# Kernel optimization log

Measured on AMD Instinct MI355X. Metric: run time of the kernel, lower is better.

Reference implementation:

```python
import jax, jax.numpy as jnp
import numpy as np

N, F = 8192, 64
SLOPE = 3.0


def _mlp(h, params):
    # params: list of (W[in,out], b[out]); Tanh after EVERY linear (incl. last)
    for W, b in params:
        h = jnp.tanh(h @ W + b)
    return h


def setup_inputs() -> dict:
    key = jax.random.key(0)
    ks = jax.random.split(key, 16)
    x = jax.random.normal(ks[0], (N, F, 2), dtype=jnp.float32)
    def lin(k, fi, fo):
        k1, k2 = jax.random.split(k)
        s = 1.0 / np.sqrt(fi)
        W = jax.random.uniform(k1, (fi, fo), jnp.float32, -s, s)
        b = jax.random.uniform(k2, (fo,), jnp.float32, -s, s)
        return W, b
    w_in1, b_in1 = lin(ks[1], 2, 4)
    w_in2, b_in2 = lin(ks[2], 4, 4)
    w_in3, b_in3 = lin(ks[3], 4, 1)
    w_a1, b_a1 = lin(ks[4], 1, 2)
    w_a2, b_a2 = lin(ks[5], 2, 1)
    w_b1, b_b1 = lin(ks[6], 1, 2)
    w_b2, b_b2 = lin(ks[7], 2, 1)
    return dict(x=x,
                w_in1=w_in1, b_in1=b_in1, w_in2=w_in2, b_in2=b_in2,
                w_in3=w_in3, b_in3=b_in3,
                w_a1=w_a1, b_a1=b_a1, w_a2=w_a2, b_a2=b_a2,
                w_b1=w_b1, b_b1=b_b1, w_b2=w_b2, b_b2=b_b2)


def reference(x, w_in1, b_in1, w_in2, b_in2, w_in3, b_in3,
              w_a1, b_a1, w_a2, b_a2, w_b1, b_b1, w_b2, b_b2):
    n, f = x.shape[0], x.shape[1]
    # per-coordinate-pair encode: [N*F,2] -> [N*F,1] -> [N,F]
    h = _mlp(x.reshape(-1, 2), [(w_in1, b_in1), (w_in2, b_in2), (w_in3, b_in3)])
    xe = h.reshape(n, f)
    # dense self-attention aggregation, softmax over dim 0 (columns normalized)
    attn = jax.nn.softmax(xe @ xe.T, axis=0)  # [N,N]
    xe = attn @ xe                            # [N,F]
    # pairwise squared euclidean distances E[i,j] = ||x_i - x_j||^2
    sq = jnp.sum(xe * xe, axis=1)             # [N]
    E = sq[:, None] + sq[None, :] - 2.0 * (xe @ xe.T)
    m = jnp.mean(E).reshape(1)                # [1]
    alpha = jnp.exp(SLOPE * _mlp(m, [(w_a1, b_a1), (w_a2, b_a2)]))
    beta = jnp.exp(-SLOPE * _mlp(m, [(w_b1, b_b1), (w_b2, b_b2)]))
    return xe, alpha, beta
```

## Files before the change

kernel.cpp:

```cpp
#include <hip/hip_runtime.h>
#include <cstdint>

typedef __bf16 bf16x8 __attribute__((ext_vector_type(8)));
typedef __bf16 bf16x4 __attribute__((ext_vector_type(4)));
typedef float  f32x4  __attribute__((ext_vector_type(4)));

#define N_PTS 8192
#define FDIM  64
#define NF    (N_PTS * FDIM)

__device__ __forceinline__ float ftanh(float x) {
    float e = __expf(2.f * x);
    return 1.f - 2.f / (e + 1.f);
}

__global__ __launch_bounds__(256) void k_encode(
    const float* __restrict__ x,
    const float* __restrict__ w1, const float* __restrict__ b1,
    const float* __restrict__ w2, const float* __restrict__ b2,
    const float* __restrict__ w3, const float* __restrict__ b3,
    __bf16* __restrict__ xe)
{
    int idx = blockIdx.x * 256 + threadIdx.x;
    float2 p = ((const float2*)x)[idx];
    float h1[4], h2[4];
#pragma unroll
    for (int o = 0; o < 4; o++)
        h1[o] = ftanh(p.x * w1[o] + p.y * w1[4 + o] + b1[o]);
#pragma unroll
    for (int o = 0; o < 4; o++) {
        float s = b2[o];
#pragma unroll
        for (int i = 0; i < 4; i++) s += h1[i] * w2[i * 4 + o];
        h2[o] = ftanh(s);
    }
    float s3 = b3[0];
#pragma unroll
    for (int i = 0; i < 4; i++) s3 += h2[i] * w3[i];
    xe[idx] = (__bf16)ftanh(s3);
}

__global__ __launch_bounds__(256) void k_pass1(
    const __bf16* __restrict__ xe, float* __restrict__ Dp)
{
    __shared__ __bf16 sI[128 * 72];
    const int tid = threadIdx.x;
    const int j0 = blockIdx.x * 64;
    const int ibase = blockIdx.y * 1024;
    const int wave = tid >> 6, lane = tid & 63, c = lane & 15, q = lane >> 4;

    bf16x8 Bf[4][2];
#pragma unroll
    for (int jt = 0; jt < 4; jt++)
#pragma unroll
        for (int kc = 0; kc < 2; kc++)
            Bf[jt][kc] = *(const bf16x8*)(xe + (j0 + 16 * jt + c) * 64 + kc * 32 + q * 8);

    float es[4] = {0.f, 0.f, 0.f, 0.f};
    for (int ic = 0; ic < 8; ic++) {
        __syncthreads();
#pragma unroll
        for (int k = 0; k < 4; k++) {
            int seg = tid + k * 256; int r = seg >> 3, c8 = seg & 7;
            *(uint4*)(sI + r * 72 + c8 * 8) =
                *(const uint4*)(xe + (ibase + ic * 128 + r) * 64 + c8 * 8);
        }
        __syncthreads();
#pragma unroll
        for (int g = 0; g < 2; g++) {
            bf16x8 a0 = *(const bf16x8*)(sI + (32 * wave + 16 * g + c) * 72 + q * 8);
            bf16x8 a1 = *(const bf16x8*)(sI + (32 * wave + 16 * g + c) * 72 + 32 + q * 8);
#pragma unroll
            for (int jt = 0; jt < 4; jt++) {
                f32x4 s = {0.f, 0.f, 0.f, 0.f};
                s = __builtin_amdgcn_mfma_f32_16x16x32_bf16(a0, Bf[jt][0], s, 0, 0, 0);
                s = __builtin_amdgcn_mfma_f32_16x16x32_bf16(a1, Bf[jt][1], s, 0, 0, 0);
                es[jt] += __expf(s.x) + __expf(s.y) + __expf(s.z) + __expf(s.w);
            }
        }
    }
#pragma unroll
    for (int jt = 0; jt < 4; jt++) {
        es[jt] += __shfl_xor(es[jt], 16);
        es[jt] += __shfl_xor(es[jt], 32);
    }
    if (q == 0) {
        float* d = Dp + (blockIdx.y * 4 + wave) * N_PTS + j0;
#pragma unroll
        for (int jt = 0; jt < 4; jt++) d[16 * jt + c] = es[jt];
    }
}

__global__ __launch_bounds__(256) void k_build_u(
    const __bf16* __restrict__ xe, const float* __restrict__ Dp,
    __bf16* __restrict__ uT)
{
    __shared__ __bf16 T[64 * 72];
    const int tid = threadIdx.x;
    const int j0 = blockIdx.x * 64;
    const int r = tid >> 2, cg = tid & 3;
    float dsum = 0.f;
#pragma unroll
    for (int s = 0; s < 32; s++) dsum += Dp[s * N_PTS + j0 + r];
    float invd = 1.0f / dsum;
    bf16x8 v0 = *(const bf16x8*)(xe + (j0 + r) * 64 + cg * 16);
    bf16x8 v1 = *(const bf16x8*)(xe + (j0 + r) * 64 + cg * 16 + 8);
#pragma unroll
    for (int e = 0; e < 8; e++) {
        T[(cg * 16 + e) * 72 + r]     = (__bf16)((float)v0[e] * invd);
        T[(cg * 16 + 8 + e) * 72 + r] = (__bf16)((float)v1[e] * invd);
    }
    __syncthreads();
    uint4 w0 = *(uint4*)((char*)T + r * 144 + cg * 32);
    uint4 w1 = *(uint4*)((char*)T + r * 144 + cg * 32 + 16);
    *(uint4*)(uT + r * 8192 + j0 + cg * 16)     = w0;
    *(uint4*)(uT + r * 8192 + j0 + cg * 16 + 8) = w1;
}

__global__ __launch_bounds__(256) void k_pass2(
    const __bf16* __restrict__ xe, const __bf16* __restrict__ uT,
    float* __restrict__ outp)
{
    __shared__ __bf16 sJ[64 * 72];
    __shared__ __bf16 sU[64 * 72];
    __shared__ __bf16 sP[128 * 72];
    const int tid = threadIdx.x;
    const int ibase = blockIdx.x * 128;
    const int jbase = blockIdx.y * 512;
    const int wave = tid >> 6, lane = tid & 63, c = lane & 15, q = lane >> 4;

    bf16x8 bst[2][2];
#pragma unroll
    for (int isub = 0; isub < 2; isub++)
#pragma unroll
        for (int kc = 0; kc < 2; kc++)
            bst[isub][kc] = *(const bf16x8*)(xe + (ibase + 32 * wave + 16 * isub + c) * 64 + kc * 32 + q * 8);

    f32x4 o[2][4];
#pragma unroll
    for (int a = 0; a < 2; a++)
#pragma unroll
        for (int b = 0; b < 4; b++) o[a][b] = (f32x4){0.f, 0.f, 0.f, 0.f};

    for (int jc = 0; jc < 8; jc++) {
        const int j0 = jbase + jc * 64;
        __syncthreads();
#pragma unroll
        for (int k = 0; k < 2; k++) {
            int seg = tid + k * 256; int r = seg >> 3, c8 = seg & 7;
            *(uint4*)(sJ + r * 72 + c8 * 8) = *(const uint4*)(xe + (j0 + r) * 64 + c8 * 8);
            *(uint4*)(sU + r * 72 + c8 * 8) = *(const uint4*)(uT + r * 8192 + j0 + c8 * 8);
        }
        __syncthreads();

#pragma unroll
        for (int jt = 0; jt < 4; jt++) {
            bf16x8 a0 = *(const bf16x8*)(sJ + (16 * jt + c) * 72 + q * 8);
            bf16x8 a1 = *(const bf16x8*)(sJ + (16 * jt + c) * 72 + 32 + q * 8);
#pragma unroll
            for (int isub = 0; isub < 2; isub++) {
                f32x4 s = {0.f, 0.f, 0.f, 0.f};
                s = __builtin_amdgcn_mfma_f32_16x16x32_bf16(a0, bst[isub][0], s, 0, 0, 0);
                s = __builtin_amdgcn_mfma_f32_16x16x32_bf16(a1, bst[isub][1], s, 0, 0, 0);
                bf16x4 pv;
                pv[0] = (__bf16)__expf(s[0]); pv[1] = (__bf16)__expf(s[1]);
                pv[2] = (__bf16)__expf(s[2]); pv[3] = (__bf16)__expf(s[3]);
                *(bf16x4*)(sP + (32 * wave + 16 * isub + c) * 72 + 16 * jt + 4 * q) = pv;
            }
        }
#pragma unroll
        for (int kc = 0; kc < 2; kc++) {
            bf16x8 ap0 = *(const bf16x8*)(sP + (32 * wave + c) * 72 + kc * 32 + q * 8);
            bf16x8 ap1 = *(const bf16x8*)(sP + (32 * wave + 16 + c) * 72 + kc * 32 + q * 8);
#pragma unroll
            for (int ft = 0; ft < 4; ft++) {
                bf16x8 bu = *(const bf16x8*)(sU + (16 * ft + c) * 72 + kc * 32 + q * 8);
                o[0][ft] = __builtin_amdgcn_mfma_f32_16x16x32_bf16(ap0, bu, o[0][ft], 0, 0, 0);
                o[1][ft] = __builtin_amdgcn_mfma_f32_16x16x32_bf16(ap1, bu, o[1][ft], 0, 0, 0);
            }
        }
    }
    float* dst = outp + (size_t)blockIdx.y * NF;
#pragma unroll
    for (int isub = 0; isub < 2; isub++)
#pragma unroll
        for (int ft = 0; ft < 4; ft++)
#pragma unroll
            for (int r = 0; r < 4; r++)
                dst[(ibase + 32 * wave + 16 * isub + 4 * q + r) * 64 + 16 * ft + c] =
                    o[isub][ft][r];
}

__global__ __launch_bounds__(256) void k_combine(
    const float* __restrict__ outp, float* __restrict__ out,
    float* __restrict__ colp, float* __restrict__ sqp)
{
    const int tid = threadIdx.x;
    const int base = blockIdx.x * 256 + tid;
    float col = 0.f, sq = 0.f;
#pragma unroll
    for (int k = 0; k < 8; k++) {
        int idx = base + k * 65536;
        float acc = 0.f;
#pragma unroll
        for (int s = 0; s < 16; s++) acc += outp[(size_t)s * NF + idx];
        out[idx] = acc;
        col += acc; sq += acc * acc;
    }
    __shared__ float sv[256];
    __shared__ float sw[4];
    sv[tid] = col;
#pragma unroll
    for (int m = 32; m; m >>= 1) sq += __shfl_xor(sq, m);
    if ((tid & 63) == 0) sw[tid >> 6] = sq;
    __syncthreads();
    if (tid < 64) {
        float t = sv[tid] + sv[tid + 64] + sv[tid + 128] + sv[tid + 192];
        colp[blockIdx.x * 64 + tid] = t;
    }
    if (tid == 0) sqp[blockIdx.x] = sw[0] + sw[1] + sw[2] + sw[3];
}

__global__ void k_final(
    const float* __restrict__ colp, const float* __restrict__ sqp,
    const float* __restrict__ wa1, const float* __restrict__ ba1,
    const float* __restrict__ wa2, const float* __restrict__ ba2,
    const float* __restrict__ wb1, const float* __restrict__ bb1,
    const float* __restrict__ wb2, const float* __restrict__ bb2,
    float* __restrict__ out_tail)
{
    const int f = threadIdx.x;
    float colsum = 0.f;
    for (int b = 0; b < 256; b++) colsum += colp[b * 64 + f];
    float ss = colsum * colsum;
#pragma unroll
    for (int m = 32; m; m >>= 1) ss += __shfl_xor(ss, m);
    float sq = 0.f;
#pragma unroll
    for (int k = 0; k < 4; k++) sq += sqp[f + 64 * k];
#pragma unroll
    for (int m = 32; m; m >>= 1) sq += __shfl_xor(sq, m);
    if (f == 0) {
        const float invN = 1.f / 8192.f;
        float m = 2.f * invN * sq - 2.f * invN * invN * ss;
        float h0 = tanhf(m * wa1[0] + ba1[0]);
        float h1 = tanhf(m * wa1[1] + ba1[1]);
        float a  = tanhf(h0 * wa2[0] + h1 * wa2[1] + ba2[0]);
        float g0 = tanhf(m * wb1[0] + bb1[0]);
        float g1 = tanhf(m * wb1[1] + bb1[1]);
        float b  = tanhf(g0 * wb2[0] + g1 * wb2[1] + bb2[0]);
        out_tail[0] = __expf(3.f * a);
        out_tail[1] = __expf(-3.f * b);
    }
}

extern "C" void kernel_launch(void* const* d_in, const int* in_sizes, int n_in,
                              void* d_out, int out_size, void* d_ws, size_t ws_size,
                              hipStream_t stream)
{
    const float* x     = (const float*)d_in[0];
    const float* w_in1 = (const float*)d_in[1];
    const float* b_in1 = (const float*)d_in[2];
    const float* w_in2 = (const float*)d_in[3];
    const float* b_in2 = (const float*)d_in[4];
    const float* w_in3 = (const float*)d_in[5];
    const float* b_in3 = (const float*)d_in[6];
    const float* w_a1  = (const float*)d_in[7];
    const float* b_a1  = (const float*)d_in[8];
    const float* w_a2  = (const float*)d_in[9];
    const float* b_a2  = (const float*)d_in[10];
    const float* w_b1  = (const float*)d_in[11];
    const float* b_b1  = (const float*)d_in[12];
    const float* w_b2  = (const float*)d_in[13];
    const float* b_b2  = (const float*)d_in[14];

    float* out = (float*)d_out;
    char*  ws  = (char*)d_ws;
    __bf16* xe  = (__bf16*)ws;
    __bf16* uT  = (__bf16*)(ws + (1 << 20));
    float*  Dp  = (float*)(ws + (2 << 20));
    float*  colp = (float*)(ws + (3 << 20));
    float*  sqp  = (float*)(ws + (3 << 20) + (1 << 16));
    float*  outp = (float*)(ws + (4 << 20));

    k_encode<<<NF / 256, 256, 0, stream>>>(x, w_in1, b_in1, w_in2, b_in2, w_in3, b_in3, xe);
    k_pass1<<<dim3(128, 8), 256, 0, stream>>>(xe, Dp);
    k_build_u<<<128, 256, 0, stream>>>(xe, Dp, uT);
    k_pass2<<<dim3(64, 16), 256, 0, stream>>>(xe, uT, outp);
    k_combine<<<256, 256, 0, stream>>>(outp, out, colp, sqp);
    k_final<<<1, 64, 0, stream>>>(colp, sqp, w_a1, b_a1, w_a2, b_a2,
                                  w_b1, b_b1, w_b2, b_b2, out + NF);
}
```

Measured before the change: 159.3 us.

## Double rows per block in pass2 to reuse staged J/U tiles

Each pass2 block now handles 256 query rows (two 128-row sub-tiles) instead of 128. The J and U tiles staged in shared memory, and their register fragments, are reused across both sub-tiles. The grid shrinks from 64x16 to 32x16 blocks, and launch bounds now request 2 blocks per CU. This halves global-to-LDS staging traffic per row and hoists the shared-memory fragment loads, at the cost of more registers (doubled accumulators) and fewer blocks (512) to fill the GPU.

```diff
diff --git a/kernel.cpp b/kernel.cpp
--- a/kernel.cpp
+++ b/kernel.cpp
@@ -117,7 +117,7 @@
     *(uint4*)(uT + r * 8192 + j0 + cg * 16 + 8) = w1;
 }
 
-__global__ __launch_bounds__(256) void k_pass2(
+__global__ __launch_bounds__(256, 2) void k_pass2(
     const __bf16* __restrict__ xe, const __bf16* __restrict__ uT,
     float* __restrict__ outp)
 {
@@ -125,22 +125,27 @@
     __shared__ __bf16 sU[64 * 72];
     __shared__ __bf16 sP[128 * 72];
     const int tid = threadIdx.x;
-    const int ibase = blockIdx.x * 128;
+    const int ibase = blockIdx.x * 256;
     const int jbase = blockIdx.y * 512;
     const int wave = tid >> 6, lane = tid & 63, c = lane & 15, q = lane >> 4;
 
-    bf16x8 bst[2][2];
-#pragma unroll
-    for (int isub = 0; isub < 2; isub++)
-#pragma unroll
-        for (int kc = 0; kc < 2; kc++)
-            bst[isub][kc] = *(const bf16x8*)(xe + (ibase + 32 * wave + 16 * isub + c) * 64 + kc * 32 + q * 8);
-
-    f32x4 o[2][4];
-#pragma unroll
-    for (int a = 0; a < 2; a++)
-#pragma unroll
-        for (int b = 0; b < 4; b++) o[a][b] = (f32x4){0.f, 0.f, 0.f, 0.f};
+    bf16x8 bst[2][2][2];
+#pragma unroll
+    for (int it = 0; it < 2; it++)
+#pragma unroll
+        for (int isub = 0; isub < 2; isub++)
+#pragma unroll
+            for (int kc = 0; kc < 2; kc++)
+                bst[it][isub][kc] = *(const bf16x8*)(
+                    xe + (ibase + it * 128 + 32 * wave + 16 * isub + c) * 64 + kc * 32 + q * 8);
+
+    f32x4 o[2][2][4];
+#pragma unroll
+    for (int it = 0; it < 2; it++)
+#pragma unroll
+        for (int g = 0; g < 2; g++)
+#pragma unroll
+            for (int ft = 0; ft < 4; ft++) o[it][g][ft] = (f32x4){0.f, 0.f, 0.f, 0.f};
 
     for (int jc = 0; jc < 8; jc++) {
         const int j0 = jbase + jc * 64;
@@ -153,42 +158,57 @@
         }
         __syncthreads();
 
-#pragma unroll
-        for (int jt = 0; jt < 4; jt++) {
-            bf16x8 a0 = *(const bf16x8*)(sJ + (16 * jt + c) * 72 + q * 8);
-            bf16x8 a1 = *(const bf16x8*)(sJ + (16 * jt + c) * 72 + 32 + q * 8);
-#pragma unroll
-            for (int isub = 0; isub < 2; isub++) {
-                f32x4 s = {0.f, 0.f, 0.f, 0.f};
-                s = __builtin_amdgcn_mfma_f32_16x16x32_bf16(a0, bst[isub][0], s, 0, 0, 0);
-                s = __builtin_amdgcn_mfma_f32_16x16x32_bf16(a1, bst[isub][1], s, 0, 0, 0);
-                bf16x4 pv;
-                pv[0] = (__bf16)__expf(s[0]); pv[1] = (__bf16)__expf(s[1]);
-                pv[2] = (__bf16)__expf(s[2]); pv[3] = (__bf16)__expf(s[3]);
-                *(bf16x4*)(sP + (32 * wave + 16 * isub + c) * 72 + 16 * jt + 4 * q) = pv;
+        bf16x8 aJ[4][2];
+#pragma unroll
+        for (int jt = 0; jt < 4; jt++)
+#pragma unroll
+            for (int kc = 0; kc < 2; kc++)
+                aJ[jt][kc] = *(const bf16x8*)(sJ + (16 * jt + c) * 72 + kc * 32 + q * 8);
+        bf16x8 bu[2][4];
+#pragma unroll
+        for (int kc = 0; kc < 2; kc++)
+#pragma unroll
+            for (int ft = 0; ft < 4; ft++)
+                bu[kc][ft] = *(const bf16x8*)(sU + (16 * ft + c) * 72 + kc * 32 + q * 8);
+
+#pragma unroll
+        for (int it = 0; it < 2; it++) {
+#pragma unroll
+            for (int jt = 0; jt < 4; jt++) {
+#pragma unroll
+                for (int isub = 0; isub < 2; isub++) {
+                    f32x4 s = {0.f, 0.f, 0.f, 0.f};
+                    s = __builtin_amdgcn_mfma_f32_16x16x32_bf16(aJ[jt][0], bst[it][isub][0], s, 0, 0, 0);
+                    s = __builtin_amdgcn_mfma_f32_16x16x32_bf16(aJ[jt][1], bst[it][isub][1], s, 0, 0, 0);
+                    bf16x4 pv;
+                    pv[0] = (__bf16)__expf(s[0]); pv[1] = (__bf16)__expf(s[1]);
+                    pv[2] = (__bf16)__expf(s[2]); pv[3] = (__bf16)__expf(s[3]);
+                    *(bf16x4*)(sP + (32 * wave + 16 * isub + c) * 72 + 16 * jt + 4 * q) = pv;
+                }
+            }
+#pragma unroll
+            for (int kc = 0; kc < 2; kc++) {
+                bf16x8 ap0 = *(const bf16x8*)(sP + (32 * wave + c) * 72 + kc * 32 + q * 8);
+                bf16x8 ap1 = *(const bf16x8*)(sP + (32 * wave + 16 + c) * 72 + kc * 32 + q * 8);
+#pragma unroll
+                for (int ft = 0; ft < 4; ft++) {
+                    o[it][0][ft] = __builtin_amdgcn_mfma_f32_16x16x32_bf16(ap0, bu[kc][ft], o[it][0][ft], 0, 0, 0);
+                    o[it][1][ft] = __builtin_amdgcn_mfma_f32_16x16x32_bf16(ap1, bu[kc][ft], o[it][1][ft], 0, 0, 0);
+                }
             }
         }
-#pragma unroll
-        for (int kc = 0; kc < 2; kc++) {
-            bf16x8 ap0 = *(const bf16x8*)(sP + (32 * wave + c) * 72 + kc * 32 + q * 8);
-            bf16x8 ap1 = *(const bf16x8*)(sP + (32 * wave + 16 + c) * 72 + kc * 32 + q * 8);
-#pragma unroll
-            for (int ft = 0; ft < 4; ft++) {
-                bf16x8 bu = *(const bf16x8*)(sU + (16 * ft + c) * 72 + kc * 32 + q * 8);
-                o[0][ft] = __builtin_amdgcn_mfma_f32_16x16x32_bf16(ap0, bu, o[0][ft], 0, 0, 0);
-                o[1][ft] = __builtin_amdgcn_mfma_f32_16x16x32_bf16(ap1, bu, o[1][ft], 0, 0, 0);
-            }
-        }
     }
     float* dst = outp + (size_t)blockIdx.y * NF;
 #pragma unroll
-    for (int isub = 0; isub < 2; isub++)
-#pragma unroll
-        for (int ft = 0; ft < 4; ft++)
-#pragma unroll
-            for (int r = 0; r < 4; r++)
-                dst[(ibase + 32 * wave + 16 * isub + 4 * q + r) * 64 + 16 * ft + c] =
-                    o[isub][ft][r];
+    for (int it = 0; it < 2; it++)
+#pragma unroll
+        for (int g = 0; g < 2; g++)
+#pragma unroll
+            for (int ft = 0; ft < 4; ft++)
+#pragma unroll
+                for (int r = 0; r < 4; r++)
+                    dst[(ibase + it * 128 + 32 * wave + 16 * g + 4 * q + r) * 64 + 16 * ft + c] =
+                        o[it][g][ft][r];
 }
 
 __global__ __launch_bounds__(256) void k_combine(
@@ -286,7 +306,7 @@
     k_encode<<<NF / 256, 256, 0, stream>>>(x, w_in1, b_in1, w_in2, b_in2, w_in3, b_in3, xe);
     k_pass1<<<dim3(128, 8), 256, 0, stream>>>(xe, Dp);
     k_build_u<<<128, 256, 0, stream>>>(xe, Dp, uT);
-    k_pass2<<<dim3(64, 16), 256, 0, stream>>>(xe, uT, outp);
+    k_pass2<<<dim3(32, 16), 256, 0, stream>>>(xe, uT, outp);
     k_combine<<<256, 256, 0, stream>>>(outp, out, colp, sqp);
     k_final<<<1, 64, 0, stream>>>(colp, sqp, w_a1, b_a1, w_a2, b_a2,
                                   w_b1, b_b1, w_b2, b_b2, out + NF);
```

After: 158.1 us. Within noise of the previous version (-0.8%).

## Fuse all stages into one cooperative persistent kernel with grid syncs

Applied to the files above, without the earlier changes.

Replaces the six separate launches with a single cooperative kernel of 512 blocks that runs encode, pass1, build_u, pass2, combine and final, separated by grid-wide barriers. The work split changes with it: pass1 uses 4 row splits instead of 8, and pass2 uses 8 column splits instead of 16, so the partial-sum buffers and combine reads shrink. The aim is to remove launch overhead and inter-kernel gaps. In exchange, each block does longer serial loops, fewer independent blocks are in flight during the heavy passes, and grid.sync adds its own cost.

```diff
diff --git a/kernel.cpp b/kernel.cpp
--- a/kernel.cpp
+++ b/kernel.cpp
@@ -1,5 +1,8 @@
 #include <hip/hip_runtime.h>
+#include <hip/hip_cooperative_groups.h>
 #include <cstdint>
+
+namespace cg = cooperative_groups;
 
 typedef __bf16 bf16x8 __attribute__((ext_vector_type(8)));
 typedef __bf16 bf16x4 __attribute__((ext_vector_type(4)));
@@ -8,249 +11,243 @@
 #define N_PTS 8192
 #define FDIM  64
 #define NF    (N_PTS * FDIM)
+
+struct Params {
+    const float *x, *w1, *b1, *w2, *b2, *w3, *b3;
+    const float *wa1, *ba1, *wa2, *ba2, *wb1, *bb1, *wb2, *bb2;
+    __bf16 *xe, *uT;
+    float *Dp, *colp, *sqp, *outp, *out;
+};
 
 __device__ __forceinline__ float ftanh(float x) {
     float e = __expf(2.f * x);
     return 1.f - 2.f / (e + 1.f);
 }
 
-__global__ __launch_bounds__(256) void k_encode(
-    const float* __restrict__ x,
-    const float* __restrict__ w1, const float* __restrict__ b1,
-    const float* __restrict__ w2, const float* __restrict__ b2,
-    const float* __restrict__ w3, const float* __restrict__ b3,
-    __bf16* __restrict__ xe)
+__global__ __launch_bounds__(256, 2) void k_mega(Params p)
 {
-    int idx = blockIdx.x * 256 + threadIdx.x;
-    float2 p = ((const float2*)x)[idx];
-    float h1[4], h2[4];
-#pragma unroll
-    for (int o = 0; o < 4; o++)
-        h1[o] = ftanh(p.x * w1[o] + p.y * w1[4 + o] + b1[o]);
-#pragma unroll
-    for (int o = 0; o < 4; o++) {
-        float s = b2[o];
-#pragma unroll
-        for (int i = 0; i < 4; i++) s += h1[i] * w2[i * 4 + o];
-        h2[o] = ftanh(s);
-    }
-    float s3 = b3[0];
-#pragma unroll
-    for (int i = 0; i < 4; i++) s3 += h2[i] * w3[i];
-    xe[idx] = (__bf16)ftanh(s3);
-}
-
-__global__ __launch_bounds__(256) void k_pass1(
-    const __bf16* __restrict__ xe, float* __restrict__ Dp)
-{
-    __shared__ __bf16 sI[128 * 72];
-    const int tid = threadIdx.x;
-    const int j0 = blockIdx.x * 64;
-    const int ibase = blockIdx.y * 1024;
+    __shared__ __bf16 smem[18432];
+    const int tid = threadIdx.x, bid = blockIdx.x;
     const int wave = tid >> 6, lane = tid & 63, c = lane & 15, q = lane >> 4;
-
-    bf16x8 Bf[4][2];
-#pragma unroll
-    for (int jt = 0; jt < 4; jt++)
-#pragma unroll
-        for (int kc = 0; kc < 2; kc++)
-            Bf[jt][kc] = *(const bf16x8*)(xe + (j0 + 16 * jt + c) * 64 + kc * 32 + q * 8);
-
-    float es[4] = {0.f, 0.f, 0.f, 0.f};
-    for (int ic = 0; ic < 8; ic++) {
+    cg::grid_group grid = cg::this_grid();
+
+    {
+#pragma unroll
+        for (int k = 0; k < 4; k++) {
+            int idx = bid * 256 + tid + k * 131072;
+            float2 pt = ((const float2*)p.x)[idx];
+            float h1[4], h2[4];
+#pragma unroll
+            for (int o = 0; o < 4; o++)
+                h1[o] = ftanh(pt.x * p.w1[o] + pt.y * p.w1[4 + o] + p.b1[o]);
+#pragma unroll
+            for (int o = 0; o < 4; o++) {
+                float s = p.b2[o];
+#pragma unroll
+                for (int i = 0; i < 4; i++) s += h1[i] * p.w2[i * 4 + o];
+                h2[o] = ftanh(s);
+            }
+            float s3 = p.b3[0];
+#pragma unroll
+            for (int i = 0; i < 4; i++) s3 += h2[i] * p.w3[i];
+            p.xe[idx] = (__bf16)ftanh(s3);
+        }
+    }
+    grid.sync();
+
+    {
+        __bf16* sI = smem;
+        const int j0 = (bid >> 2) * 64;
+        const int ibase = (bid & 3) * 2048;
+
+        bf16x8 Bf[4][2];
+#pragma unroll
+        for (int jt = 0; jt < 4; jt++)
+#pragma unroll
+            for (int kc = 0; kc < 2; kc++)
+                Bf[jt][kc] = *(const bf16x8*)(p.xe + (j0 + 16 * jt + c) * 64 + kc * 32 + q * 8);
+
+        float es[4] = {0.f, 0.f, 0.f, 0.f};
+        for (int ic = 0; ic < 16; ic++) {
+            __syncthreads();
+#pragma unroll
+            for (int k = 0; k < 4; k++) {
+                int seg = tid + k * 256; int r = seg >> 3, c8 = seg & 7;
+                *(uint4*)(sI + r * 72 + c8 * 8) =
+                    *(const uint4*)(p.xe + (ibase + ic * 128 + r) * 64 + c8 * 8);
+            }
+            __syncthreads();
+#pragma unroll
+            for (int g = 0; g < 2; g++) {
+                bf16x8 a0 = *(const bf16x8*)(sI + (32 * wave + 16 * g + c) * 72 + q * 8);
+                bf16x8 a1 = *(const bf16x8*)(sI + (32 * wave + 16 * g + c) * 72 + 32 + q * 8);
+#pragma unroll
+                for (int jt = 0; jt < 4; jt++) {
+                    f32x4 s = {0.f, 0.f, 0.f, 0.f};
+                    s = __builtin_amdgcn_mfma_f32_16x16x32_bf16(a0, Bf[jt][0], s, 0, 0, 0);
+                    s = __builtin_amdgcn_mfma_f32_16x16x32_bf16(a1, Bf[jt][1], s, 0, 0, 0);
+                    es[jt] += __expf(s.x) + __expf(s.y) + __expf(s.z) + __expf(s.w);
+                }
+            }
+        }
+#pragma unroll
+        for (int jt = 0; jt < 4; jt++) {
+            es[jt] += __shfl_xor(es[jt], 16);
+            es[jt] += __shfl_xor(es[jt], 32);
+        }
+        if (q == 0) {
+            float* d = p.Dp + ((bid & 3) * 4 + wave) * N_PTS + j0;
+#pragma unroll
+            for (int jt = 0; jt < 4; jt++) d[16 * jt + c] = es[jt];
+        }
+    }
+    grid.sync();
+
+    if (bid < 128) {
+        __bf16* T = smem;
+        const int j0 = bid * 64;
+        const int r = tid >> 2, cg4 = tid & 3;
+        float dsum = 0.f;
+#pragma unroll
+        for (int s = 0; s < 16; s++) dsum += p.Dp[s * N_PTS + j0 + r];
+        float invd = 1.0f / dsum;
+        bf16x8 v0 = *(const bf16x8*)(p.xe + (j0 + r) * 64 + cg4 * 16);
+        bf16x8 v1 = *(const bf16x8*)(p.xe + (j0 + r) * 64 + cg4 * 16 + 8);
+#pragma unroll
+        for (int e = 0; e < 8; e++) {
+            T[(cg4 * 16 + e) * 72 + r]     = (__bf16)((float)v0[e] * invd);
+            T[(cg4 * 16 + 8 + e) * 72 + r] = (__bf16)((float)v1[e] * invd);
+        }
         __syncthreads();
+        uint4 w0 = *(uint4*)((char*)T + r * 144 + cg4 * 32);
+        uint4 w1 = *(uint4*)((char*)T + r * 144 + cg4 * 32 + 16);
+        *(uint4*)(p.uT + r * 8192 + j0 + cg4 * 16)     = w0;
+        *(uint4*)(p.uT + r * 8192 + j0 + cg4 * 16 + 8) = w1;
+    }
+    grid.sync();
+
+    {
+        __bf16* sJ = smem;
+        __bf16* sU = smem + 4608;
+        __bf16* sP = smem + 9216;
+        const int ibase = (bid >> 3) * 128;
+        const int jbase = (bid & 7) * 1024;
+
+        bf16x8 bst[2][2];
+#pragma unroll
+        for (int isub = 0; isub < 2; isub++)
+#pragma unroll
+            for (int kc = 0; kc < 2; kc++)
+                bst[isub][kc] = *(const bf16x8*)(
+                    p.xe + (ibase + 32 * wave + 16 * isub + c) * 64 + kc * 32 + q * 8);
+
+        f32x4 o[2][4];
+#pragma unroll
+        for (int g = 0; g < 2; g++)
+#pragma unroll
+            for (int ft = 0; ft < 4; ft++) o[g][ft] = (f32x4){0.f, 0.f, 0.f, 0.f};
+
+        for (int jc = 0; jc < 16; jc++) {
+            const int j0 = jbase + jc * 64;
+            __syncthreads();
+#pragma unroll
+            for (int k = 0; k < 2; k++) {
+                int seg = tid + k * 256; int r = seg >> 3, c8 = seg & 7;
+                *(uint4*)(sJ + r * 72 + c8 * 8) = *(const uint4*)(p.xe + (j0 + r) * 64 + c8 * 8);
+                *(uint4*)(sU + r * 72 + c8 * 8) = *(const uint4*)(p.uT + r * 8192 + j0 + c8 * 8);
+            }
+            __syncthreads();
+
+#pragma unroll
+            for (int jt = 0; jt < 4; jt++) {
+                bf16x8 a0 = *(const bf16x8*)(sJ + (16 * jt + c) * 72 + q * 8);
+                bf16x8 a1 = *(const bf16x8*)(sJ + (16 * jt + c) * 72 + 32 + q * 8);
+#pragma unroll
+                for (int isub = 0; isub < 2; isub++) {
+                    f32x4 s = {0.f, 0.f, 0.f, 0.f};
+                    s = __builtin_amdgcn_mfma_f32_16x16x32_bf16(a0, bst[isub][0], s, 0, 0, 0);
+                    s = __builtin_amdgcn_mfma_f32_16x16x32_bf16(a1, bst[isub][1], s, 0, 0, 0);
+                    bf16x4 pv;
+                    pv[0] = (__bf16)__expf(s[0]); pv[1] = (__bf16)__expf(s[1]);
+                    pv[2] = (__bf16)__expf(s[2]); pv[3] = (__bf16)__expf(s[3]);
+                    *(bf16x4*)(sP + (32 * wave + 16 * isub + c) * 72 + 16 * jt + 4 * q) = pv;
+                }
+            }
+#pragma unroll
+            for (int kc = 0; kc < 2; kc++) {
+                bf16x8 ap0 = *(const bf16x8*)(sP + (32 * wave + c) * 72 + kc * 32 + q * 8);
+                bf16x8 ap1 = *(const bf16x8*)(sP + (32 * wave + 16 + c) * 72 + kc * 32 + q * 8);
+#pragma unroll
+                for (int ft = 0; ft < 4; ft++) {
+                    bf16x8 bu = *(const bf16x8*)(sU + (16 * ft + c) * 72 + kc * 32 + q * 8);
+                    o[0][ft] = __builtin_amdgcn_mfma_f32_16x16x32_bf16(ap0, bu, o[0][ft], 0, 0, 0);
+                    o[1][ft] = __builtin_amdgcn_mfma_f32_16x16x32_bf16(ap1, bu, o[1][ft], 0, 0, 0);
+                }
+            }
+        }
+        float* dst = p.outp + (size_t)(bid & 7) * NF;
+#pragma unroll
+        for (int g = 0; g < 2; g++)
+#pragma unroll
+            for (int ft = 0; ft < 4; ft++)
+#pragma unroll
+                for (int r = 0; r < 4; r++)
+                    dst[(ibase + 32 * wave + 16 * g + 4 * q + r) * 64 + 16 * ft + c] =
+                        o[g][ft][r];
+    }
+    grid.sync();
+
+    {
+        float* svf = (float*)smem;
+        float* swf = svf + 256;
+        const int base = bid * 256 + tid;
+        float col = 0.f, sq = 0.f;
 #pragma unroll
         for (int k = 0; k < 4; k++) {
-            int seg = tid + k * 256; int r = seg >> 3, c8 = seg & 7;
-            *(uint4*)(sI + r * 72 + c8 * 8) =
-                *(const uint4*)(xe + (ibase + ic * 128 + r) * 64 + c8 * 8);
-        }
+            int idx = base + k * 131072;
+            float acc = 0.f;
+#pragma unroll
+            for (int s = 0; s < 8; s++) acc += p.outp[(size_t)s * NF + idx];
+            p.out[idx] = acc;
+            col += acc; sq += acc * acc;
+        }
+        svf[tid] = col;
+#pragma unroll
+        for (int m = 32; m; m >>= 1) sq += __shfl_xor(sq, m);
+        if ((tid & 63) == 0) swf[tid >> 6] = sq;
         __syncthreads();
-#pragma unroll
-        for (int g = 0; g < 2; g++) {
-            bf16x8 a0 = *(const bf16x8*)(sI + (32 * wave + 16 * g + c) * 72 + q * 8);
-            bf16x8 a1 = *(const bf16x8*)(sI + (32 * wave + 16 * g + c) * 72 + 32 + q * 8);
-#pragma unroll
-            for (int jt = 0; jt < 4; jt++) {
-                f32x4 s = {0.f, 0.f, 0.f, 0.f};
-                s = __builtin_amdgcn_mfma_f32_16x16x32_bf16(a0, Bf[jt][0], s, 0, 0, 0);
-                s = __builtin_amdgcn_mfma_f32_16x16x32_bf16(a1, Bf[jt][1], s, 0, 0, 0);
-                es[jt] += __expf(s.x) + __expf(s.y) + __expf(s.z) + __expf(s.w);
-            }
-        }
-    }
-#pragma unroll
-    for (int jt = 0; jt < 4; jt++) {
-        es[jt] += __shfl_xor(es[jt], 16);
-        es[jt] += __shfl_xor(es[jt], 32);
-    }
-    if (q == 0) {
-        float* d = Dp + (blockIdx.y * 4 + wave) * N_PTS + j0;
-#pragma unroll
-        for (int jt = 0; jt < 4; jt++) d[16 * jt + c] = es[jt];
-    }
-}
-
-__global__ __launch_bounds__(256) void k_build_u(
-    const __bf16* __restrict__ xe, const float* __restrict__ Dp,
-    __bf16* __restrict__ uT)
-{
-    __shared__ __bf16 T[64 * 72];
-    const int tid = threadIdx.x;
-    const int j0 = blockIdx.x * 64;
-    const int r = tid >> 2, cg = tid & 3;
-    float dsum = 0.f;
-#pragma unroll
-    for (int s = 0; s < 32; s++) dsum += Dp[s * N_PTS + j0 + r];
-    float invd = 1.0f / dsum;
-    bf16x8 v0 = *(const bf16x8*)(xe + (j0 + r) * 64 + cg * 16);
-    bf16x8 v1 = *(const bf16x8*)(xe + (j0 + r) * 64 + cg * 16 + 8);
-#pragma unroll
-    for (int e = 0; e < 8; e++) {
-        T[(cg * 16 + e) * 72 + r]     = (__bf16)((float)v0[e] * invd);
-        T[(cg * 16 + 8 + e) * 72 + r] = (__bf16)((float)v1[e] * invd);
-    }
-    __syncthreads();
-    uint4 w0 = *(uint4*)((char*)T + r * 144 + cg * 32);
-    uint4 w1 = *(uint4*)((char*)T + r * 144 + cg * 32 + 16);
-    *(uint4*)(uT + r * 8192 + j0 + cg * 16)     = w0;
-    *(uint4*)(uT + r * 8192 + j0 + cg * 16 + 8) = w1;
-}
-
-__global__ __launch_bounds__(256) void k_pass2(
-    const __bf16* __restrict__ xe, const __bf16* __restrict__ uT,
-    float* __restrict__ outp)
-{
-    __shared__ __bf16 sJ[64 * 72];
-    __shared__ __bf16 sU[64 * 72];
-    __shared__ __bf16 sP[128 * 72];
-    const int tid = threadIdx.x;
-    const int ibase = blockIdx.x * 128;
-    const int jbase = blockIdx.y * 512;
-    const int wave = tid >> 6, lane = tid & 63, c = lane & 15, q = lane >> 4;
-
-    bf16x8 bst[2][2];
-#pragma unroll
-    for (int isub = 0; isub < 2; isub++)
-#pragma unroll
-        for (int kc = 0; kc < 2; kc++)
-            bst[isub][kc] = *(const bf16x8*)(xe + (ibase + 32 * wave + 16 * isub + c) * 64 + kc * 32 + q * 8);
-
-    f32x4 o[2][4];
-#pragma unroll
-    for (int a = 0; a < 2; a++)
-#pragma unroll
-        for (int b = 0; b < 4; b++) o[a][b] = (f32x4){0.f, 0.f, 0.f, 0.f};
-
-    for (int jc = 0; jc < 8; jc++) {
-        const int j0 = jbase + jc * 64;
-        __syncthreads();
-#pragma unroll
-        for (int k = 0; k < 2; k++) {
-            int seg = tid + k * 256; int r = seg >> 3, c8 = seg & 7;
-            *(uint4*)(sJ + r * 72 + c8 * 8) = *(const uint4*)(xe + (j0 + r) * 64 + c8 * 8);
-            *(uint4*)(sU + r * 72 + c8 * 8) = *(const uint4*)(uT + r * 8192 + j0 + c8 * 8);
-        }
-        __syncthreads();
-
-#pragma unroll
-        for (int jt = 0; jt < 4; jt++) {
-            bf16x8 a0 = *(const bf16x8*)(sJ + (16 * jt + c) * 72 + q * 8);
-            bf16x8 a1 = *(const bf16x8*)(sJ + (16 * jt + c) * 72 + 32 + q * 8);
-#pragma unroll
-            for (int isub = 0; isub < 2; isub++) {
-                f32x4 s = {0.f, 0.f, 0.f, 0.f};
-                s = __builtin_amdgcn_mfma_f32_16x16x32_bf16(a0, bst[isub][0], s, 0, 0, 0);
-                s = __builtin_amdgcn_mfma_f32_16x16x32_bf16(a1, bst[isub][1], s, 0, 0, 0);
-                bf16x4 pv;
-                pv[0] = (__bf16)__expf(s[0]); pv[1] = (__bf16)__expf(s[1]);
-                pv[2] = (__bf16)__expf(s[2]); pv[3] = (__bf16)__expf(s[3]);
-                *(bf16x4*)(sP + (32 * wave + 16 * isub + c) * 72 + 16 * jt + 4 * q) = pv;
-            }
-        }
-#pragma unroll
-        for (int kc = 0; kc < 2; kc++) {
-            bf16x8 ap0 = *(const bf16x8*)(sP + (32 * wave + c) * 72 + kc * 32 + q * 8);
-            bf16x8 ap1 = *(const bf16x8*)(sP + (32 * wave + 16 + c) * 72 + kc * 32 + q * 8);
-#pragma unroll
-            for (int ft = 0; ft < 4; ft++) {
-                bf16x8 bu = *(const bf16x8*)(sU + (16 * ft + c) * 72 + kc * 32 + q * 8);
-                o[0][ft] = __builtin_amdgcn_mfma_f32_16x16x32_bf16(ap0, bu, o[0][ft], 0, 0, 0);
-                o[1][ft] = __builtin_amdgcn_mfma_f32_16x16x32_bf16(ap1, bu, o[1][ft], 0, 0, 0);
-            }
-        }
-    }
-    float* dst = outp + (size_t)blockIdx.y * NF;
-#pragma unroll
-    for (int isub = 0; isub < 2; isub++)
-#pragma unroll
-        for (int ft = 0; ft < 4; ft++)
-#pragma unroll
-            for (int r = 0; r < 4; r++)
-                dst[(ibase + 32 * wave + 16 * isub + 4 * q + r) * 64 + 16 * ft + c] =
-                    o[isub][ft][r];
-}
-
-__global__ __launch_bounds__(256) void k_combine(
-    const float* __restrict__ outp, float* __restrict__ out,
-    float* __restrict__ colp, float* __restrict__ sqp)
-{
-    const int tid = threadIdx.x;
-    const int base = blockIdx.x * 256 + tid;
-    float col = 0.f, sq = 0.f;
-#pragma unroll
-    for (int k = 0; k < 8; k++) {
-        int idx = base + k * 65536;
-        float acc = 0.f;
-#pragma unroll
-        for (int s = 0; s < 16; s++) acc += outp[(size_t)s * NF + idx];
-        out[idx] = acc;
-        col += acc; sq += acc * acc;
-    }
-    __shared__ float sv[256];
-    __shared__ float sw[4];
-    sv[tid] = col;
-#pragma unroll
-    for (int m = 32; m; m >>= 1) sq += __shfl_xor(sq, m);
-    if ((tid & 63) == 0) sw[tid >> 6] = sq;
-    __syncthreads();
-    if (tid < 64) {
-        float t = sv[tid] + sv[tid + 64] + sv[tid + 128] + sv[tid + 192];
-        colp[blockIdx.x * 64 + tid] = t;
-    }
-    if (tid == 0) sqp[blockIdx.x] = sw[0] + sw[1] + sw[2] + sw[3];
-}
-
-__global__ void k_final(
-    const float* __restrict__ colp, const float* __restrict__ sqp,
-    const float* __restrict__ wa1, const float* __restrict__ ba1,
-    const float* __restrict__ wa2, const float* __restrict__ ba2,
-    const float* __restrict__ wb1, const float* __restrict__ bb1,
-    const float* __restrict__ wb2, const float* __restrict__ bb2,
-    float* __restrict__ out_tail)
-{
-    const int f = threadIdx.x;
-    float colsum = 0.f;
-    for (int b = 0; b < 256; b++) colsum += colp[b * 64 + f];
-    float ss = colsum * colsum;
-#pragma unroll
-    for (int m = 32; m; m >>= 1) ss += __shfl_xor(ss, m);
-    float sq = 0.f;
-#pragma unroll
-    for (int k = 0; k < 4; k++) sq += sqp[f + 64 * k];
-#pragma unroll
-    for (int m = 32; m; m >>= 1) sq += __shfl_xor(sq, m);
-    if (f == 0) {
-        const float invN = 1.f / 8192.f;
-        float m = 2.f * invN * sq - 2.f * invN * invN * ss;
-        float h0 = tanhf(m * wa1[0] + ba1[0]);
-        float h1 = tanhf(m * wa1[1] + ba1[1]);
-        float a  = tanhf(h0 * wa2[0] + h1 * wa2[1] + ba2[0]);
-        float g0 = tanhf(m * wb1[0] + bb1[0]);
-        float g1 = tanhf(m * wb1[1] + bb1[1]);
-        float b  = tanhf(g0 * wb2[0] + g1 * wb2[1] + bb2[0]);
-        out_tail[0] = __expf(3.f * a);
-        out_tail[1] = __expf(-3.f * b);
+        if (tid < 64) {
+            float t = svf[tid] + svf[tid + 64] + svf[tid + 128] + svf[tid + 192];
+            p.colp[bid * 64 + tid] = t;
+        }
+        if (tid == 0) p.sqp[bid] = swf[0] + swf[1] + swf[2] + swf[3];
+    }
+    grid.sync();
+
+    if (bid == 0 && tid < 64) {
+        const int f = tid;
+        float colsum = 0.f;
+        for (int b = 0; b < 512; b++) colsum += p.colp[b * 64 + f];
+        float ss = colsum * colsum;
+#pragma unroll
+        for (int m = 32; m; m >>= 1) ss += __shfl_xor(ss, m);
+        float sq = 0.f;
+#pragma unroll
+        for (int k = 0; k < 8; k++) sq += p.sqp[f + 64 * k];
+#pragma unroll
+        for (int m = 32; m; m >>= 1) sq += __shfl_xor(sq, m);
+        if (f == 0) {
+            const float invN = 1.f / 8192.f;
+            float m = 2.f * invN * sq - 2.f * invN * invN * ss;
+            float h0 = tanhf(m * p.wa1[0] + p.ba1[0]);
+            float h1 = tanhf(m * p.wa1[1] + p.ba1[1]);
+            float a  = tanhf(h0 * p.wa2[0] + h1 * p.wa2[1] + p.ba2[0]);
+            float g0 = tanhf(m * p.wb1[0] + p.bb1[0]);
+            float g1 = tanhf(m * p.wb1[1] + p.bb1[1]);
+            float b  = tanhf(g0 * p.wb2[0] + g1 * p.wb2[1] + p.bb2[0]);
+            p.out[NF]     = __expf(3.f * a);
+            p.out[NF + 1] = __expf(-3.f * b);
+        }
     }
 }
 
@@ -258,36 +255,25 @@
                               void* d_out, int out_size, void* d_ws, size_t ws_size,
                               hipStream_t stream)
 {
-    const float* x     = (const float*)d_in[0];
-    const float* w_in1 = (const float*)d_in[1];
-    const float* b_in1 = (const float*)d_in[2];
-    const float* w_in2 = (const float*)d_in[3];
-    const float* b_in2 = (const float*)d_in[4];
-    const float* w_in3 = (const float*)d_in[5];
-    const float* b_in3 = (const float*)d_in[6];
-    const float* w_a1  = (const float*)d_in[7];
-    const float* b_a1  = (const float*)d_in[8];
-    const float* w_a2  = (const float*)d_in[9];
-    const float* b_a2  = (const float*)d_in[10];
-    const float* w_b1  = (const float*)d_in[11];
-    const float* b_b1  = (const float*)d_in[12];
-    const float* w_b2  = (const float*)d_in[13];
-    const float* b_b2  = (const float*)d_in[14];
-
-    float* out = (float*)d_out;
-    char*  ws  = (char*)d_ws;
-    __bf16* xe  = (__bf16*)ws;
-    __bf16* uT  = (__bf16*)(ws + (1 << 20));
-    float*  Dp  = (float*)(ws + (2 << 20));
-    float*  colp = (float*)(ws + (3 << 20));
-    float*  sqp  = (float*)(ws + (3 << 20) + (1 << 16));
-    float*  outp = (float*)(ws + (4 << 20));
-
-    k_encode<<<NF / 256, 256, 0, stream>>>(x, w_in1, b_in1, w_in2, b_in2, w_in3, b_in3, xe);
-    k_pass1<<<dim3(128, 8), 256, 0, stream>>>(xe, Dp);
-    k_build_u<<<128, 256, 0, stream>>>(xe, Dp, uT);
-    k_pass2<<<dim3(64, 16), 256, 0, stream>>>(xe, uT, outp);
-    k_combine<<<256, 256, 0, stream>>>(outp, out, colp, sqp);
-    k_final<<<1, 64, 0, stream>>>(colp, sqp, w_a1, b_a1, w_a2, b_a2,
-                                  w_b1, b_b1, w_b2, b_b2, out + NF);
+    char* ws = (char*)d_ws;
+    Params prm;
+    prm.x   = (const float*)d_in[0];
+    prm.w1  = (const float*)d_in[1];  prm.b1  = (const float*)d_in[2];
+    prm.w2  = (const float*)d_in[3];  prm.b2  = (const float*)d_in[4];
+    prm.w3  = (const float*)d_in[5];  prm.b3  = (const float*)d_in[6];
+    prm.wa1 = (const float*)d_in[7];  prm.ba1 = (const float*)d_in[8];
+    prm.wa2 = (const float*)d_in[9];  prm.ba2 = (const float*)d_in[10];
+    prm.wb1 = (const float*)d_in[11]; prm.bb1 = (const float*)d_in[12];
+    prm.wb2 = (const float*)d_in[13]; prm.bb2 = (const float*)d_in[14];
+    prm.xe  = (__bf16*)ws;
+    prm.uT  = (__bf16*)(ws + (1 << 20));
+    prm.Dp  = (float*)(ws + (2 << 20));
+    prm.colp = (float*)(ws + (2 << 20) + (512 << 10));
+    prm.sqp  = (float*)(ws + (2 << 20) + (640 << 10));
+    prm.outp = (float*)(ws + (4 << 20));
+    prm.out  = (float*)d_out;
+
+    void* kargs[] = { (void*)&prm };
+    hipLaunchCooperativeKernel((void*)k_mega, dim3(512), dim3(256),
+                               kargs, 0, stream);
 }
```

Result: slower. 459.8 us (+188.6%).

## Halve pass2 j-splits, fuse final reduction into combine via last-block atomic

Applied to the files above, without the earlier changes.

Pass2 now covers 1024 columns per block across 8 y-splits instead of 16, which halves the partial output buffer the combine kernel must read. The combine kernel now runs 512 blocks, and the last block to finish, found with an atomic counter that the encode kernel resets, performs the final mean/MLP reduction. This removes the separate k_final launch. It adds launch_bounds occupancy hints, but pass2 now has 512 blocks, which may leave the GPU's compute units less fully occupied.

```diff
diff --git a/kernel.cpp b/kernel.cpp
--- a/kernel.cpp
+++ b/kernel.cpp
@@ -19,8 +19,9 @@
     const float* __restrict__ w1, const float* __restrict__ b1,
     const float* __restrict__ w2, const float* __restrict__ b2,
     const float* __restrict__ w3, const float* __restrict__ b3,
-    __bf16* __restrict__ xe)
-{
+    __bf16* __restrict__ xe, int* __restrict__ ctix)
+{
+    if (blockIdx.x == 0 && threadIdx.x == 0) *ctix = 0;
     int idx = blockIdx.x * 256 + threadIdx.x;
     float2 p = ((const float2*)x)[idx];
     float h1[4], h2[4];
@@ -117,7 +118,7 @@
     *(uint4*)(uT + r * 8192 + j0 + cg * 16 + 8) = w1;
 }
 
-__global__ __launch_bounds__(256) void k_pass2(
+__global__ __launch_bounds__(256, 2) void k_pass2(
     const __bf16* __restrict__ xe, const __bf16* __restrict__ uT,
     float* __restrict__ outp)
 {
@@ -126,7 +127,7 @@
     __shared__ __bf16 sP[128 * 72];
     const int tid = threadIdx.x;
     const int ibase = blockIdx.x * 128;
-    const int jbase = blockIdx.y * 512;
+    const int jbase = blockIdx.y * 1024;
     const int wave = tid >> 6, lane = tid & 63, c = lane & 15, q = lane >> 4;
 
     bf16x8 bst[2][2];
@@ -134,15 +135,16 @@
     for (int isub = 0; isub < 2; isub++)
 #pragma unroll
         for (int kc = 0; kc < 2; kc++)
-            bst[isub][kc] = *(const bf16x8*)(xe + (ibase + 32 * wave + 16 * isub + c) * 64 + kc * 32 + q * 8);
+            bst[isub][kc] = *(const bf16x8*)(
+                xe + (ibase + 32 * wave + 16 * isub + c) * 64 + kc * 32 + q * 8);
 
     f32x4 o[2][4];
 #pragma unroll
-    for (int a = 0; a < 2; a++)
-#pragma unroll
-        for (int b = 0; b < 4; b++) o[a][b] = (f32x4){0.f, 0.f, 0.f, 0.f};
-
-    for (int jc = 0; jc < 8; jc++) {
+    for (int g = 0; g < 2; g++)
+#pragma unroll
+        for (int ft = 0; ft < 4; ft++) o[g][ft] = (f32x4){0.f, 0.f, 0.f, 0.f};
+
+    for (int jc = 0; jc < 16; jc++) {
         const int j0 = jbase + jc * 64;
         __syncthreads();
 #pragma unroll
@@ -182,33 +184,38 @@
     }
     float* dst = outp + (size_t)blockIdx.y * NF;
 #pragma unroll
-    for (int isub = 0; isub < 2; isub++)
+    for (int g = 0; g < 2; g++)
 #pragma unroll
         for (int ft = 0; ft < 4; ft++)
 #pragma unroll
             for (int r = 0; r < 4; r++)
-                dst[(ibase + 32 * wave + 16 * isub + 4 * q + r) * 64 + 16 * ft + c] =
-                    o[isub][ft][r];
+                dst[(ibase + 32 * wave + 16 * g + 4 * q + r) * 64 + 16 * ft + c] =
+                    o[g][ft][r];
 }
 
 __global__ __launch_bounds__(256) void k_combine(
     const float* __restrict__ outp, float* __restrict__ out,
-    float* __restrict__ colp, float* __restrict__ sqp)
-{
-    const int tid = threadIdx.x;
-    const int base = blockIdx.x * 256 + tid;
+    float* __restrict__ colp, float* __restrict__ sqp, int* __restrict__ ctix,
+    const float* __restrict__ wa1, const float* __restrict__ ba1,
+    const float* __restrict__ wa2, const float* __restrict__ ba2,
+    const float* __restrict__ wb1, const float* __restrict__ bb1,
+    const float* __restrict__ wb2, const float* __restrict__ bb2)
+{
+    const int tid = threadIdx.x, bid = blockIdx.x;
+    const int base = bid * 256 + tid;
     float col = 0.f, sq = 0.f;
 #pragma unroll
-    for (int k = 0; k < 8; k++) {
-        int idx = base + k * 65536;
+    for (int k = 0; k < 4; k++) {
+        int idx = base + k * 131072;
         float acc = 0.f;
 #pragma unroll
-        for (int s = 0; s < 16; s++) acc += outp[(size_t)s * NF + idx];
+        for (int s = 0; s < 8; s++) acc += outp[(size_t)s * NF + idx];
         out[idx] = acc;
         col += acc; sq += acc * acc;
     }
     __shared__ float sv[256];
     __shared__ float sw[4];
+    __shared__ int isLast;
     sv[tid] = col;
 #pragma unroll
     for (int m = 32; m; m >>= 1) sq += __shfl_xor(sq, m);
@@ -216,41 +223,39 @@
     __syncthreads();
     if (tid < 64) {
         float t = sv[tid] + sv[tid + 64] + sv[tid + 128] + sv[tid + 192];
-        colp[blockIdx.x * 64 + tid] = t;
-    }
-    if (tid == 0) sqp[blockIdx.x] = sw[0] + sw[1] + sw[2] + sw[3];
-}
-
-__global__ void k_final(
-    const float* __restrict__ colp, const float* __restrict__ sqp,
-    const float* __restrict__ wa1, const float* __restrict__ ba1,
-    const float* __restrict__ wa2, const float* __restrict__ ba2,
-    const float* __restrict__ wb1, const float* __restrict__ bb1,
-    const float* __restrict__ wb2, const float* __restrict__ bb2,
-    float* __restrict__ out_tail)
-{
-    const int f = threadIdx.x;
-    float colsum = 0.f;
-    for (int b = 0; b < 256; b++) colsum += colp[b * 64 + f];
-    float ss = colsum * colsum;
-#pragma unroll
-    for (int m = 32; m; m >>= 1) ss += __shfl_xor(ss, m);
-    float sq = 0.f;
-#pragma unroll
-    for (int k = 0; k < 4; k++) sq += sqp[f + 64 * k];
-#pragma unroll
-    for (int m = 32; m; m >>= 1) sq += __shfl_xor(sq, m);
-    if (f == 0) {
-        const float invN = 1.f / 8192.f;
-        float m = 2.f * invN * sq - 2.f * invN * invN * ss;
-        float h0 = tanhf(m * wa1[0] + ba1[0]);
-        float h1 = tanhf(m * wa1[1] + ba1[1]);
-        float a  = tanhf(h0 * wa2[0] + h1 * wa2[1] + ba2[0]);
-        float g0 = tanhf(m * wb1[0] + bb1[0]);
-        float g1 = tanhf(m * wb1[1] + bb1[1]);
-        float b  = tanhf(g0 * wb2[0] + g1 * wb2[1] + bb2[0]);
-        out_tail[0] = __expf(3.f * a);
-        out_tail[1] = __expf(-3.f * b);
+        colp[bid * 64 + tid] = t;
+    }
+    if (tid == 0) sqp[bid] = sw[0] + sw[1] + sw[2] + sw[3];
+
+    __threadfence();
+    if (tid == 0) isLast = (atomicAdd(ctix, 1) == 511);
+    __syncthreads();
+    if (!isLast) return;
+    __threadfence();
+    if (tid < 64) {
+        const int f = tid;
+        float colsum = 0.f;
+        for (int b = 0; b < 512; b++) colsum += colp[b * 64 + f];
+        float ss = colsum * colsum;
+#pragma unroll
+        for (int m = 32; m; m >>= 1) ss += __shfl_xor(ss, m);
+        float sqt = 0.f;
+#pragma unroll
+        for (int k = 0; k < 8; k++) sqt += sqp[f + 64 * k];
+#pragma unroll
+        for (int m = 32; m; m >>= 1) sqt += __shfl_xor(sqt, m);
+        if (f == 0) {
+            const float invN = 1.f / 8192.f;
+            float m = 2.f * invN * sqt - 2.f * invN * invN * ss;
+            float h0 = tanhf(m * wa1[0] + ba1[0]);
+            float h1 = tanhf(m * wa1[1] + ba1[1]);
+            float a  = tanhf(h0 * wa2[0] + h1 * wa2[1] + ba2[0]);
+            float g0 = tanhf(m * wb1[0] + bb1[0]);
+            float g1 = tanhf(m * wb1[1] + bb1[1]);
+            float b  = tanhf(g0 * wb2[0] + g1 * wb2[1] + bb2[0]);
+            out[NF]     = __expf(3.f * a);
+            out[NF + 1] = __expf(-3.f * b);
+        }
     }
 }
 
@@ -280,14 +285,16 @@
     __bf16* uT  = (__bf16*)(ws + (1 << 20));
     float*  Dp  = (float*)(ws + (2 << 20));
     float*  colp = (float*)(ws + (3 << 20));
-    float*  sqp  = (float*)(ws + (3 << 20) + (1 << 16));
+    float*  sqp  = (float*)(ws + (3 << 20) + (128 << 10));
+    int*    ctix = (int*)(ws + (3 << 20) + (130 << 10));
     float*  outp = (float*)(ws + (4 << 20));
 
-    k_encode<<<NF / 256, 256, 0, stream>>>(x, w_in1, b_in1, w_in2, b_in2, w_in3, b_in3, xe);
+    k_encode<<<NF / 256, 256, 0, stream>>>(x, w_in1, b_in1, w_in2, b_in2,
+                                           w_in3, b_in3, xe, ctix);
     k_pass1<<<dim3(128, 8), 256, 0, stream>>>(xe, Dp);
     k_build_u<<<128, 256, 0, stream>>>(xe, Dp, uT);
-    k_pass2<<<dim3(64, 16), 256, 0, stream>>>(xe, uT, outp);
-    k_combine<<<256, 256, 0, stream>>>(outp, out, colp, sqp);
-    k_final<<<1, 64, 0, stream>>>(colp, sqp, w_a1, b_a1, w_a2, b_a2,
-                                  w_b1, b_b1, w_b2, b_b2, out + NF);
-}
+    k_pass2<<<dim3(64, 8), 256, 0, stream>>>(xe, uT, outp);
+    k_combine<<<512, 256, 0, stream>>>(outp, out, colp, sqp, ctix,
+                                       w_a1, b_a1, w_a2, b_a2,
+                                       w_b1, b_b1, w_b2, b_b2);
+}
```

Result: slower. 205.7 us (+29.1%).
